# Kernel tuning notes

Hardware: AMD Instinct MI355X
Metric: run time of the kernel (lower is better)

The kernel has to match this reference:

```python
import jax, jax.numpy as jnp
import numpy as np

B, T, D, I, E, R = 4, 2048, 2048, 6144, 8, 32


def setup_inputs() -> dict:
    key = jax.random.key(0)
    ks = jax.random.split(key, 9)
    return {
        "x": jax.random.normal(ks[0], (B, T, D), jnp.float32),
        "router_w": jax.random.normal(ks[1], (D, E), jnp.float32) * 0.02,
        "A_gate": jax.random.normal(ks[2], (E, D, R), jnp.float32) * 0.01,
        "B_gate": jax.random.normal(ks[3], (E, R, I), jnp.float32) * 0.01,
        "A_up": jax.random.normal(ks[4], (E, D, R), jnp.float32) * 0.01,
        "B_up": jax.random.normal(ks[5], (E, R, I), jnp.float32) * 0.01,
        "W_gate": jax.random.normal(ks[6], (D, I), jnp.float32) * 0.02,
        "W_up": jax.random.normal(ks[7], (D, I), jnp.float32) * 0.02,
        "W_down": jax.random.normal(ks[8], (I, D), jnp.float32) * 0.02,
    }


def reference(x, router_w, A_gate, B_gate, A_up, B_up, W_gate, W_up, W_down):
    b, t, d = x.shape
    flat = x.reshape(b * t, d)                     # [N, D]
    # Router: top-1 expert per token (argmax matches torch argmax: first max)
    gate_logits = flat @ router_w                  # [N, E]
    idx = jnp.argmax(gate_logits, axis=-1)         # [N]
    n_exp = router_w.shape[1]

    def routed_lora(A, Bm):
        # sum_e mask_e * (x @ A_e @ B_e); loop over small static expert count
        out = jnp.zeros((flat.shape[0], Bm.shape[2]), flat.dtype)
        for e in range(n_exp):
            m = (idx == e)[:, None]
            out = out + jnp.where(m, (flat @ A[e]) @ Bm[e], 0.0)
        return out

    # ExpertLoRA forward: base gate/up + per-token-selected LoRA delta, SwiGLU, down
    gate = flat @ W_gate + routed_lora(A_gate, B_gate)   # [N, I]
    up = flat @ W_up + routed_lora(A_up, B_up)           # [N, I]
    down = (jax.nn.silu(gate) * up) @ W_down             # [N, D]
    return down.reshape(b, t, d), gate_logits
```

## Files before the change

kernel.cpp:

```cpp
#include <hip/hip_runtime.h>
#include <stdint.h>

#define N_TOK 8192
#define DDIM 2048
#define IDIM 6144
#define NEXP 8
#define RLORA 32
#define NCHUNK 64
#define CHUNK 128

typedef __attribute__((ext_vector_type(8))) short short8;
typedef __attribute__((ext_vector_type(4))) float floatx4;
typedef __attribute__((ext_vector_type(4))) unsigned short ushortx4;

__device__ __forceinline__ unsigned short f2bf(float f) {
  union { float f; unsigned u; } v; v.f = f;
  unsigned u = v.u;
  unsigned r = (u + 0x7fffu + ((u >> 16) & 1u)) >> 16;
  return (unsigned short)r;
}
__device__ __forceinline__ float bf2f(unsigned short s) {
  union { unsigned u; float f; } v; v.u = ((unsigned)s) << 16;
  return v.f;
}

__device__ __forceinline__ void gload_lds16(const void* g, void* l) {
  __builtin_amdgcn_global_load_lds(
      (const __attribute__((address_space(1))) void*)g,
      (__attribute__((address_space(3))) void*)l, 16, 0, 0);
}

__global__ __launch_bounds__(256) void router_kernel(
    const float* __restrict__ x, const float* __restrict__ rw,
    float* __restrict__ logits_out, int* __restrict__ idx) {
  int wave = threadIdx.x >> 6, lane = threadIdx.x & 63;
  int n = blockIdx.x * 4 + wave;
  const float* xr = x + (size_t)n * DDIM;
  float acc[NEXP];
#pragma unroll
  for (int e = 0; e < NEXP; e++) acc[e] = 0.f;
#pragma unroll
  for (int j = 0; j < 8; j++) {
    int d = j * 256 + lane * 4;
    floatx4 v = *(const floatx4*)(xr + d);
    const float* rwd = rw + (size_t)d * NEXP;
#pragma unroll
    for (int t = 0; t < 4; t++) {
      float xv = v[t];
      const float* rr = rwd + t * NEXP;
#pragma unroll
      for (int e = 0; e < NEXP; e++) acc[e] += xv * rr[e];
    }
  }
#pragma unroll
  for (int off = 32; off > 0; off >>= 1) {
#pragma unroll
    for (int e = 0; e < NEXP; e++) acc[e] += __shfl_xor(acc[e], off, 64);
  }
  if (lane == 0) {
    float best = acc[0]; int bi = 0;
#pragma unroll
    for (int e = 1; e < NEXP; e++)
      if (acc[e] > best) { best = acc[e]; bi = e; }
    idx[n] = bi;
#pragma unroll
    for (int e = 0; e < NEXP; e++) logits_out[(size_t)n * NEXP + e] = acc[e];
  }
}

__global__ __launch_bounds__(128) void count_kernel(
    const int* __restrict__ idx, int* __restrict__ cnt) {
  __shared__ int h[NEXP];
  if (threadIdx.x < NEXP) h[threadIdx.x] = 0;
  __syncthreads();
  int n = blockIdx.x * CHUNK + threadIdx.x;
  atomicAdd(&h[idx[n]], 1);
  __syncthreads();
  if (threadIdx.x < NEXP) cnt[blockIdx.x * NEXP + threadIdx.x] = h[threadIdx.x];
}

__global__ __launch_bounds__(64) void scan_kernel(
    const int* __restrict__ cnt, int* __restrict__ off) {
  __shared__ int tot[NEXP], base[NEXP];
  int t = threadIdx.x;
  if (t < NEXP) {
    int s = 0;
    for (int c = 0; c < NCHUNK; c++) s += cnt[c * NEXP + t];
    tot[t] = s;
  }
  __syncthreads();
  if (t == 0) {
    int run = 0;
    for (int e = 0; e < NEXP; e++) { base[e] = run; run += tot[e]; }
  }
  __syncthreads();
  if (t < NEXP) {
    int run = base[t];
    for (int c = 0; c < NCHUNK; c++) { off[c * NEXP + t] = run; run += cnt[c * NEXP + t]; }
  }
}

__global__ __launch_bounds__(64) void rank_kernel(
    const int* __restrict__ idx, const int* __restrict__ off,
    int* __restrict__ sortpos, int* __restrict__ orig, int* __restrict__ eidx) {
  if (threadIdx.x != 0) return;
  int c = blockIdx.x;
  int lc[NEXP];
#pragma unroll
  for (int e = 0; e < NEXP; e++) lc[e] = 0;
  for (int t = 0; t < CHUNK; t++) {
    int n = c * CHUNK + t;
    int e = idx[n];
    int dst = off[c * NEXP + e] + lc[e]++;
    sortpos[n] = dst;
    orig[dst] = n;
    eidx[dst] = e;
  }
}

__global__ __launch_bounds__(256) void permute_x_kernel(
    const float* __restrict__ x, const int* __restrict__ sortpos,
    unsigned short* __restrict__ xb) {
  int wave = threadIdx.x >> 6, lane = threadIdx.x & 63;
  int n = blockIdx.x * 4 + wave;
  int dst = sortpos[n];
  const float* xr = x + (size_t)n * DDIM;
  unsigned short* xbr = xb + (size_t)dst * DDIM;
#pragma unroll
  for (int j = 0; j < 8; j++) {
    int d = j * 256 + lane * 4;
    floatx4 v = *(const floatx4*)(xr + d);
    ushortx4 s;
    s[0] = f2bf(v[0]); s[1] = f2bf(v[1]); s[2] = f2bf(v[2]); s[3] = f2bf(v[3]);
    *(ushortx4*)(xbr + d) = s;
  }
}

__global__ __launch_bounds__(256) void transpose_w_kernel(
    const float* __restrict__ in, unsigned short* __restrict__ out, int Rr, int Cc) {
  __shared__ float lds[32][33];
  int r0 = blockIdx.y * 32, c0 = blockIdx.x * 32;
  int tx = threadIdx.x & 31, ty = threadIdx.x >> 5;
#pragma unroll
  for (int k = 0; k < 4; k++) {
    int r = ty + k * 8;
    lds[r][tx] = in[(size_t)(r0 + r) * Cc + c0 + tx];
  }
  __syncthreads();
#pragma unroll
  for (int k = 0; k < 4; k++) {
    int cc = ty + k * 8;
    out[(size_t)(c0 + cc) * Rr + r0 + tx] = f2bf(lds[tx][cc]);
  }
}

__global__ __launch_bounds__(256) void pack_a_kernel(
    const float* __restrict__ Ag, const float* __restrict__ Au,
    unsigned short* __restrict__ aat) {
  int o = blockIdx.x * 256 + threadIdx.x;
  int h = o >> 19;
  int oo = o & ((1 << 19) - 1);
  int c = oo >> 11, d = oo & 2047;
  int e = c >> 5, r = c & 31;
  const float* src = h ? Au : Ag;
  float v = src[(e << 16) + (d << 5) + r];
  aat[(size_t)(h * 256 + c) * DDIM + d] = f2bf(v);
}

__global__ __launch_bounds__(256) void transpose_b_kernel(
    const float* __restrict__ Bg, const float* __restrict__ Bu,
    unsigned short* __restrict__ btg, unsigned short* __restrict__ btu) {
  __shared__ float lds[32][33];
  int i0 = blockIdx.x * 32, e = blockIdx.y;
  const float* in = blockIdx.z ? Bu : Bg;
  unsigned short* out = blockIdx.z ? btu : btg;
  int tx = threadIdx.x & 31, ty = threadIdx.x >> 5;
#pragma unroll
  for (int k = 0; k < 4; k++) {
    int r = ty + k * 8;
    lds[r][tx] = in[((size_t)e * RLORA + r) * IDIM + i0 + tx];
  }
  __syncthreads();
#pragma unroll
  for (int k = 0; k < 4; k++) {
    int ii = ty + k * 8;
    out[((size_t)e * IDIM + i0 + ii) * RLORA + tx] = f2bf(lds[tx][ii]);
  }
}

__global__ __launch_bounds__(256) void gemm_tsel_kernel(
    const unsigned short* __restrict__ xb, const unsigned short* __restrict__ aat,
    const int* __restrict__ eidx, unsigned short* __restrict__ Tsel) {
  __shared__ __align__(16) unsigned short sA[4096], sB[2048];
  __shared__ int es_s[128];
  const int row0 = blockIdx.x * 128;
  const int tid = threadIdx.x;
  const int wave = tid >> 6, lane = tid & 63;
  const int wr = wave >> 1, wc = wave & 1;
  const int q = lane >> 4, m16 = lane & 15;
  if (tid < 128) es_s[tid] = eidx[row0 + tid];
  __syncthreads();
  const int emin = es_s[0], emax = es_s[127];
  int erow[4];
#pragma unroll
  for (int m = 0; m < 4; m++) erow[m] = es_s[wr * 64 + m * 16 + m16];
  floatx4 acc[8];
#pragma unroll
  for (int i = 0; i < 8; i++)
#pragma unroll
    for (int j = 0; j < 4; j++) acc[i][j] = 0.f;
  short8 zero;
#pragma unroll
  for (int i = 0; i < 8; i++) zero[i] = 0;
  for (int ee = emin; ee <= emax; ee++) {
    for (int k0 = 0; k0 < DDIM; k0 += 32) {
      __syncthreads();
#pragma unroll
      for (int rr = 0; rr < 2; rr++) {
        int e = tid * 8 + rr * 2048;
        int r = e >> 5, kk = e & 31;
        gload_lds16(xb + (size_t)(row0 + r) * DDIM + (k0 + kk), sA + e);
      }
      {
        int e2 = tid * 8;
        int c = e2 >> 5, kk = e2 & 31;
        int srow = (c < 32) ? (ee * 32 + c) : (256 + ee * 32 + (c - 32));
        gload_lds16(aat + (size_t)srow * DDIM + (k0 + kk), sB + e2);
      }
      __syncthreads();
      short8 a[4], b[2];
#pragma unroll
      for (int m = 0; m < 4; m++) {
        short8 av = *(const short8*)(sA + (wr * 64 + m * 16 + m16) * 32 + q * 8);
        a[m] = (erow[m] == ee) ? av : zero;
      }
#pragma unroll
      for (int n = 0; n < 2; n++)
        b[n] = *(const short8*)(sB + (wc * 32 + n * 16 + m16) * 32 + q * 8);
#pragma unroll
      for (int m = 0; m < 4; m++)
#pragma unroll
        for (int n = 0; n < 2; n++)
          acc[m * 2 + n] = __builtin_amdgcn_mfma_f32_16x16x32_bf16(a[m], b[n], acc[m * 2 + n], 0, 0, 0);
    }
  }
#pragma unroll
  for (int m = 0; m < 4; m++)
#pragma unroll
    for (int n = 0; n < 2; n++)
#pragma unroll
      for (int r = 0; r < 4; r++) {
        int grow = row0 + wr * 64 + m * 16 + q * 4 + r;
        int gcol = wc * 32 + n * 16 + m16;
        Tsel[(size_t)grow * 64 + gcol] = f2bf(acc[m * 2 + n][r]);
      }
}

__device__ __forceinline__ void mm_main(const unsigned short* __restrict__ Ab,
                                        const unsigned short* __restrict__ Bb,
                                        int K, int row0, int col0,
                                        unsigned short* sA, unsigned short* sB,
                                        floatx4* acc) {
  const int tid = threadIdx.x;
  const int wave = tid >> 6, lane = tid & 63;
  const int wr = wave >> 1, wc = wave & 1;
  const int q = lane >> 4, m16 = lane & 15;
  for (int k0 = 0; k0 < K; k0 += 32) {
    __syncthreads();
#pragma unroll
    for (int rr = 0; rr < 2; rr++) {
      int e = tid * 8 + rr * 2048;
      int r = e >> 5, kk = e & 31;
      gload_lds16(Ab + (size_t)(row0 + r) * K + (k0 + kk), sA + e);
      gload_lds16(Bb + (size_t)(col0 + r) * K + (k0 + kk), sB + e);
    }
    __syncthreads();
    short8 a[4], b[4];
#pragma unroll
    for (int m = 0; m < 4; m++)
      a[m] = *(const short8*)(sA + (wr * 64 + m * 16 + m16) * 32 + q * 8);
#pragma unroll
    for (int n = 0; n < 4; n++)
      b[n] = *(const short8*)(sB + (wc * 64 + n * 16 + m16) * 32 + q * 8);
#pragma unroll
    for (int m = 0; m < 4; m++)
#pragma unroll
      for (int n = 0; n < 4; n++)
        acc[m * 4 + n] = __builtin_amdgcn_mfma_f32_16x16x32_bf16(a[m], b[n], acc[m * 4 + n], 0, 0, 0);
  }
}

__device__ __forceinline__ void lora_epilogue(const unsigned short* __restrict__ Tsel,
                                              const unsigned short* __restrict__ Bt,
                                              const int* __restrict__ eidx,
                                              int half, int row0, int col0,
                                              unsigned short* sA, unsigned short* sB,
                                              int* es_s, floatx4* acc) {
  const int tid = threadIdx.x;
  const int wave = tid >> 6, lane = tid & 63;
  const int wr = wave >> 1, wc = wave & 1;
  const int q = lane >> 4, m16 = lane & 15;
  __syncthreads();
  if (tid < 128) es_s[tid] = eidx[row0 + tid];
#pragma unroll
  for (int rr = 0; rr < 2; rr++) {
    int e = tid * 8 + rr * 2048;
    int r = e >> 5, kk = e & 31;
    *(floatx4*)(sA + e) = *(const floatx4*)(Tsel + (size_t)(row0 + r) * 64 + half * 32 + kk);
  }
  __syncthreads();
  const int emin = es_s[0], emax = es_s[127];
  short8 ta[4]; int erow[4];
#pragma unroll
  for (int m = 0; m < 4; m++) {
    int rloc = wr * 64 + m * 16 + m16;
    ta[m] = *(const short8*)(sA + rloc * 32 + q * 8);
    erow[m] = es_s[rloc];
  }
  short8 zero;
#pragma unroll
  for (int i = 0; i < 8; i++) zero[i] = 0;
  for (int ee = emin; ee <= emax; ee++) {
    __syncthreads();
#pragma unroll
    for (int rr = 0; rr < 2; rr++) {
      int e2 = tid * 8 + rr * 2048;
      int c = e2 >> 5, kk = e2 & 31;
      *(floatx4*)(sB + e2) = *(const floatx4*)(Bt + ((size_t)ee * IDIM + col0 + c) * RLORA + kk);
    }
    __syncthreads();
    short8 bfr[4];
#pragma unroll
    for (int n = 0; n < 4; n++)
      bfr[n] = *(const short8*)(sB + (wc * 64 + n * 16 + m16) * 32 + q * 8);
#pragma unroll
    for (int m = 0; m < 4; m++) {
      short8 am = (erow[m] == ee) ? ta[m] : zero;
#pragma unroll
      for (int n = 0; n < 4; n++)
        acc[m * 4 + n] = __builtin_amdgcn_mfma_f32_16x16x32_bf16(am, bfr[n], acc[m * 4 + n], 0, 0, 0);
    }
  }
}

__device__ __forceinline__ void swizzle_gu(int lin, int& bx, int& by) {
  int xcd = lin & 7, slot = lin >> 3;
  bx = xcd * 6 + slot % 6;
  by = slot / 6;
}

__global__ __launch_bounds__(256) void gemm_gate_kernel(
    const unsigned short* __restrict__ xb, const unsigned short* __restrict__ wgt,
    const unsigned short* __restrict__ Tsel, const unsigned short* __restrict__ btg,
    const int* __restrict__ eidx, unsigned short* __restrict__ gbuf) {
  __shared__ __align__(16) unsigned short sA[4096], sB[4096];
  __shared__ int es_s[128];
  floatx4 acc[16];
#pragma unroll
  for (int i = 0; i < 16; i++)
#pragma unroll
    for (int j = 0; j < 4; j++) acc[i][j] = 0.f;
  int bx, by; swizzle_gu(blockIdx.x, bx, by);
  int row0 = by * 128, col0 = bx * 128;
  mm_main(xb, wgt, DDIM, row0, col0, sA, sB, acc);
  lora_epilogue(Tsel, btg, eidx, 0, row0, col0, sA, sB, es_s, acc);
  const int wave = threadIdx.x >> 6, lane = threadIdx.x & 63;
  const int wr = wave >> 1, wc = wave & 1;
  const int q = lane >> 4, m16 = lane & 15;
#pragma unroll
  for (int m = 0; m < 4; m++)
#pragma unroll
    for (int n = 0; n < 4; n++)
#pragma unroll
      for (int r = 0; r < 4; r++) {
        int grow = row0 + wr * 64 + m * 16 + q * 4 + r;
        int gcol = col0 + wc * 64 + n * 16 + m16;
        gbuf[(size_t)grow * IDIM + gcol] = f2bf(acc[m * 4 + n][r]);
      }
}

__global__ __launch_bounds__(256) void gemm_up_kernel(
    const unsigned short* __restrict__ xb, const unsigned short* __restrict__ wut,
    const unsigned short* __restrict__ Tsel, const unsigned short* __restrict__ btu,
    const int* __restrict__ eidx, unsigned short* __restrict__ gbuf) {
  __shared__ __align__(16) unsigned short sA[4096], sB[4096];
  __shared__ int es_s[128];
  floatx4 acc[16];
#pragma unroll
  for (int i = 0; i < 16; i++)
#pragma unroll
    for (int j = 0; j < 4; j++) acc[i][j] = 0.f;
  int bx, by; swizzle_gu(blockIdx.x, bx, by);
  int row0 = by * 128, col0 = bx * 128;
  mm_main(xb, wut, DDIM, row0, col0, sA, sB, acc);
  lora_epilogue(Tsel, btu, eidx, 1, row0, col0, sA, sB, es_s, acc);
  const int wave = threadIdx.x >> 6, lane = threadIdx.x & 63;
  const int wr = wave >> 1, wc = wave & 1;
  const int q = lane >> 4, m16 = lane & 15;
#pragma unroll
  for (int m = 0; m < 4; m++)
#pragma unroll
    for (int n = 0; n < 4; n++)
#pragma unroll
      for (int r = 0; r < 4; r++) {
        int grow = row0 + wr * 64 + m * 16 + q * 4 + r;
        int gcol = col0 + wc * 64 + n * 16 + m16;
        size_t o = (size_t)grow * IDIM + gcol;
        float gv = bf2f(gbuf[o]);
        float hv = gv / (1.f + __expf(-gv)) * acc[m * 4 + n][r];
        gbuf[o] = f2bf(hv);
      }
}

__global__ __launch_bounds__(256) void gemm_down_kernel(
    const unsigned short* __restrict__ hb, const unsigned short* __restrict__ wdt,
    const int* __restrict__ orig, float* __restrict__ out) {
  __shared__ __align__(16) unsigned short sA[4096], sB[4096];
  floatx4 acc[16];
#pragma unroll
  for (int i = 0; i < 16; i++)
#pragma unroll
    for (int j = 0; j < 4; j++) acc[i][j] = 0.f;
  int lin = blockIdx.x;
  int xcd = lin & 7, slot = lin >> 3;
  int bx = xcd * 2 + (slot & 1);
  int by = slot >> 1;
  int row0 = by * 128, col0 = bx * 128;
  mm_main(hb, wdt, IDIM, row0, col0, sA, sB, acc);
  const int wave = threadIdx.x >> 6, lane = threadIdx.x & 63;
  const int wr = wave >> 1, wc = wave & 1;
  const int q = lane >> 4, m16 = lane & 15;
#pragma unroll
  for (int m = 0; m < 4; m++)
#pragma unroll
    for (int n = 0; n < 4; n++)
#pragma unroll
      for (int r = 0; r < 4; r++) {
        int grow = row0 + wr * 64 + m * 16 + q * 4 + r;
        int orow = orig[grow];
        int gcol = col0 + wc * 64 + n * 16 + m16;
        out[(size_t)orow * DDIM + gcol] = acc[m * 4 + n][r];
      }
}

extern "C" void kernel_launch(void* const* d_in, const int* in_sizes, int n_in,
                              void* d_out, int out_size, void* d_ws, size_t ws_size,
                              hipStream_t stream) {
  const float* x  = (const float*)d_in[0];
  const float* rw = (const float*)d_in[1];
  const float* Ag = (const float*)d_in[2];
  const float* Bg = (const float*)d_in[3];
  const float* Au = (const float*)d_in[4];
  const float* Bu = (const float*)d_in[5];
  const float* Wg = (const float*)d_in[6];
  const float* Wu = (const float*)d_in[7];
  const float* Wd = (const float*)d_in[8];
  float* out = (float*)d_out;
  float* logits = out + (size_t)N_TOK * DDIM;

  char* ws = (char*)d_ws;
  size_t off = 0;
  auto alloc = [&](size_t bytes) {
    char* p = ws + off;
    off += (bytes + 255) & ~(size_t)255;
    return p;
  };
  unsigned short* xb  = (unsigned short*)alloc((size_t)N_TOK * DDIM * 2);
  unsigned short* wgt = (unsigned short*)alloc((size_t)IDIM * DDIM * 2);
  unsigned short* wut = (unsigned short*)alloc((size_t)IDIM * DDIM * 2);
  unsigned short* wdt = (unsigned short*)alloc((size_t)DDIM * IDIM * 2);
  unsigned short* aat = (unsigned short*)alloc((size_t)512 * DDIM * 2);
  unsigned short* btg = (unsigned short*)alloc((size_t)NEXP * IDIM * RLORA * 2);
  unsigned short* btu = (unsigned short*)alloc((size_t)NEXP * IDIM * RLORA * 2);
  unsigned short* Tsel= (unsigned short*)alloc((size_t)N_TOK * 64 * 2);
  unsigned short* gbuf= (unsigned short*)alloc((size_t)N_TOK * IDIM * 2);
  int* idx     = (int*)alloc((size_t)N_TOK * 4);
  int* sortpos = (int*)alloc((size_t)N_TOK * 4);
  int* orig    = (int*)alloc((size_t)N_TOK * 4);
  int* eidx    = (int*)alloc((size_t)N_TOK * 4);
  int* cnt     = (int*)alloc((size_t)NCHUNK * NEXP * 4);
  int* offb    = (int*)alloc((size_t)NCHUNK * NEXP * 4);

  router_kernel<<<N_TOK / 4, 256, 0, stream>>>(x, rw, logits, idx);
  count_kernel<<<NCHUNK, 128, 0, stream>>>(idx, cnt);
  scan_kernel<<<1, 64, 0, stream>>>(cnt, offb);
  rank_kernel<<<NCHUNK, 64, 0, stream>>>(idx, offb, sortpos, orig, eidx);
  permute_x_kernel<<<N_TOK / 4, 256, 0, stream>>>(x, sortpos, xb);
  transpose_w_kernel<<<dim3(IDIM / 32, DDIM / 32), 256, 0, stream>>>(Wg, wgt, DDIM, IDIM);
  transpose_w_kernel<<<dim3(IDIM / 32, DDIM / 32), 256, 0, stream>>>(Wu, wut, DDIM, IDIM);
  transpose_w_kernel<<<dim3(DDIM / 32, IDIM / 32), 256, 0, stream>>>(Wd, wdt, IDIM, DDIM);
  pack_a_kernel<<<4096, 256, 0, stream>>>(Ag, Au, aat);
  transpose_b_kernel<<<dim3(IDIM / 32, NEXP, 2), 256, 0, stream>>>(Bg, Bu, btg, btu);
  gemm_tsel_kernel<<<N_TOK / 128, 256, 0, stream>>>(xb, aat, eidx, Tsel);
  gemm_gate_kernel<<<(IDIM / 128) * (N_TOK / 128), 256, 0, stream>>>(xb, wgt, Tsel, btg, eidx, gbuf);
  gemm_up_kernel<<<(IDIM / 128) * (N_TOK / 128), 256, 0, stream>>>(xb, wut, Tsel, btu, eidx, gbuf);
  gemm_down_kernel<<<(DDIM / 128) * (N_TOK / 128), 256, 0, stream>>>(gbuf, wdt, orig, out);
}
```

Baseline: 1.238 ms.

## Fuse gate and up GEMMs with LoRA and SwiGLU into one kernel

Replaces the separate gate and up GEMM kernels with one kernel. Each 128x64 output tile computes both gate and up accumulators from a shared x tile, applies the routed LoRA deltas for both, and writes silu(gate)*up directly. This removes the bf16 round-trip of the gate intermediate through global memory and halves the x-tile loads. The cost is more registers per thread and narrower N tiles, with launch_bounds set to allow 3 blocks per CU.

Result: no change. 1.215 ms (-1.9%).

```diff
diff --git a/kernel.cpp b/kernel.cpp
--- a/kernel.cpp
+++ b/kernel.cpp
@@ -18,10 +18,6 @@
   unsigned u = v.u;
   unsigned r = (u + 0x7fffu + ((u >> 16) & 1u)) >> 16;
   return (unsigned short)r;
-}
-__device__ __forceinline__ float bf2f(unsigned short s) {
-  union { unsigned u; float f; } v; v.u = ((unsigned)s) << 16;
-  return v.f;
 }
 
 __device__ __forceinline__ void gload_lds16(const void* g, void* l) {
@@ -256,6 +252,133 @@
       }
 }
 
+__global__ __launch_bounds__(256, 3) void gemm_gateup_kernel(
+    const unsigned short* __restrict__ xb, const unsigned short* __restrict__ wgt,
+    const unsigned short* __restrict__ wut, const unsigned short* __restrict__ Tsel,
+    const unsigned short* __restrict__ btg, const unsigned short* __restrict__ btu,
+    const int* __restrict__ eidx, unsigned short* __restrict__ hbuf) {
+  __shared__ __align__(16) unsigned short smem[12288];
+  __shared__ int es_s[128];
+  unsigned short* sA  = smem;
+  unsigned short* sBg = smem + 4096;
+  unsigned short* sBu = smem + 6144;
+  unsigned short* sTg = smem;
+  unsigned short* sTu = smem + 4096;
+  unsigned short* sbg = smem + 8192;
+  unsigned short* sbu = smem + 10240;
+
+  floatx4 accg[8], accu[8];
+#pragma unroll
+  for (int i = 0; i < 8; i++)
+#pragma unroll
+    for (int j = 0; j < 4; j++) { accg[i][j] = 0.f; accu[i][j] = 0.f; }
+
+  int lin = blockIdx.x;
+  int xcd = lin & 7, slot = lin >> 3;
+  int grp = slot >> 8, sub = slot & 255;
+  int bx = xcd * 12 + grp * 4 + (sub & 3);
+  int by = sub >> 2;
+  const int row0 = by * 128, col0 = bx * 64;
+
+  const int tid = threadIdx.x;
+  const int wave = tid >> 6, lane = tid & 63;
+  const int wr = wave >> 1, wc = wave & 1;
+  const int q = lane >> 4, m16 = lane & 15;
+
+  for (int k0 = 0; k0 < DDIM; k0 += 32) {
+    __syncthreads();
+#pragma unroll
+    for (int rr = 0; rr < 2; rr++) {
+      int e = tid * 8 + rr * 2048;
+      int r = e >> 5, kk = e & 31;
+      gload_lds16(xb + (size_t)(row0 + r) * DDIM + (k0 + kk), sA + e);
+    }
+    {
+      int e2 = tid * 8;
+      int c = e2 >> 5, kk = e2 & 31;
+      gload_lds16(wgt + (size_t)(col0 + c) * DDIM + (k0 + kk), sBg + e2);
+      gload_lds16(wut + (size_t)(col0 + c) * DDIM + (k0 + kk), sBu + e2);
+    }
+    __syncthreads();
+    short8 a[4], bg[2], bu[2];
+#pragma unroll
+    for (int m = 0; m < 4; m++)
+      a[m] = *(const short8*)(sA + (wr * 64 + m * 16 + m16) * 32 + q * 8);
+#pragma unroll
+    for (int n = 0; n < 2; n++) {
+      bg[n] = *(const short8*)(sBg + (wc * 32 + n * 16 + m16) * 32 + q * 8);
+      bu[n] = *(const short8*)(sBu + (wc * 32 + n * 16 + m16) * 32 + q * 8);
+    }
+#pragma unroll
+    for (int m = 0; m < 4; m++)
+#pragma unroll
+      for (int n = 0; n < 2; n++) {
+        accg[m * 2 + n] = __builtin_amdgcn_mfma_f32_16x16x32_bf16(a[m], bg[n], accg[m * 2 + n], 0, 0, 0);
+        accu[m * 2 + n] = __builtin_amdgcn_mfma_f32_16x16x32_bf16(a[m], bu[n], accu[m * 2 + n], 0, 0, 0);
+      }
+  }
+
+  __syncthreads();
+  if (tid < 128) es_s[tid] = eidx[row0 + tid];
+#pragma unroll
+  for (int rr = 0; rr < 2; rr++) {
+    int e = tid * 8 + rr * 2048;
+    int r = e >> 5, kk = e & 31;
+    *(floatx4*)(sTg + e) = *(const floatx4*)(Tsel + (size_t)(row0 + r) * 64 + kk);
+    *(floatx4*)(sTu + e) = *(const floatx4*)(Tsel + (size_t)(row0 + r) * 64 + 32 + kk);
+  }
+  __syncthreads();
+  const int emin = es_s[0], emax = es_s[127];
+  int erow[4];
+#pragma unroll
+  for (int m = 0; m < 4; m++) erow[m] = es_s[wr * 64 + m * 16 + m16];
+  short8 zero;
+#pragma unroll
+  for (int i = 0; i < 8; i++) zero[i] = 0;
+  for (int ee = emin; ee <= emax; ee++) {
+    __syncthreads();
+    {
+      int e2 = tid * 8;
+      int c = e2 >> 5, kk = e2 & 31;
+      *(floatx4*)(sbg + e2) = *(const floatx4*)(btg + ((size_t)ee * IDIM + col0 + c) * RLORA + kk);
+      *(floatx4*)(sbu + e2) = *(const floatx4*)(btu + ((size_t)ee * IDIM + col0 + c) * RLORA + kk);
+    }
+    __syncthreads();
+    short8 bg[2], bu[2], tg[4], tu[4];
+#pragma unroll
+    for (int n = 0; n < 2; n++) {
+      bg[n] = *(const short8*)(sbg + (wc * 32 + n * 16 + m16) * 32 + q * 8);
+      bu[n] = *(const short8*)(sbu + (wc * 32 + n * 16 + m16) * 32 + q * 8);
+    }
+#pragma unroll
+    for (int m = 0; m < 4; m++) {
+      int rloc = wr * 64 + m * 16 + m16;
+      tg[m] = (erow[m] == ee) ? *(const short8*)(sTg + rloc * 32 + q * 8) : zero;
+      tu[m] = (erow[m] == ee) ? *(const short8*)(sTu + rloc * 32 + q * 8) : zero;
+    }
+#pragma unroll
+    for (int m = 0; m < 4; m++)
+#pragma unroll
+      for (int n = 0; n < 2; n++) {
+        accg[m * 2 + n] = __builtin_amdgcn_mfma_f32_16x16x32_bf16(tg[m], bg[n], accg[m * 2 + n], 0, 0, 0);
+        accu[m * 2 + n] = __builtin_amdgcn_mfma_f32_16x16x32_bf16(tu[m], bu[n], accu[m * 2 + n], 0, 0, 0);
+      }
+  }
+
+#pragma unroll
+  for (int m = 0; m < 4; m++)
+#pragma unroll
+    for (int n = 0; n < 2; n++)
+#pragma unroll
+      for (int r = 0; r < 4; r++) {
+        int grow = row0 + wr * 64 + m * 16 + q * 4 + r;
+        int gcol = col0 + wc * 32 + n * 16 + m16;
+        float gv = accg[m * 2 + n][r];
+        float hv = gv / (1.f + __expf(-gv)) * accu[m * 2 + n][r];
+        hbuf[(size_t)grow * IDIM + gcol] = f2bf(hv);
+      }
+}
+
 __device__ __forceinline__ void mm_main(const unsigned short* __restrict__ Ab,
                                         const unsigned short* __restrict__ Bb,
                                         int K, int row0, int col0,
@@ -288,128 +411,6 @@
       for (int n = 0; n < 4; n++)
         acc[m * 4 + n] = __builtin_amdgcn_mfma_f32_16x16x32_bf16(a[m], b[n], acc[m * 4 + n], 0, 0, 0);
   }
-}
-
-__device__ __forceinline__ void lora_epilogue(const unsigned short* __restrict__ Tsel,
-                                              const unsigned short* __restrict__ Bt,
-                                              const int* __restrict__ eidx,
-                                              int half, int row0, int col0,
-                                              unsigned short* sA, unsigned short* sB,
-                                              int* es_s, floatx4* acc) {
-  const int tid = threadIdx.x;
-  const int wave = tid >> 6, lane = tid & 63;
-  const int wr = wave >> 1, wc = wave & 1;
-  const int q = lane >> 4, m16 = lane & 15;
-  __syncthreads();
-  if (tid < 128) es_s[tid] = eidx[row0 + tid];
-#pragma unroll
-  for (int rr = 0; rr < 2; rr++) {
-    int e = tid * 8 + rr * 2048;
-    int r = e >> 5, kk = e & 31;
-    *(floatx4*)(sA + e) = *(const floatx4*)(Tsel + (size_t)(row0 + r) * 64 + half * 32 + kk);
-  }
-  __syncthreads();
-  const int emin = es_s[0], emax = es_s[127];
-  short8 ta[4]; int erow[4];
-#pragma unroll
-  for (int m = 0; m < 4; m++) {
-    int rloc = wr * 64 + m * 16 + m16;
-    ta[m] = *(const short8*)(sA + rloc * 32 + q * 8);
-    erow[m] = es_s[rloc];
-  }
-  short8 zero;
-#pragma unroll
-  for (int i = 0; i < 8; i++) zero[i] = 0;
-  for (int ee = emin; ee <= emax; ee++) {
-    __syncthreads();
-#pragma unroll
-    for (int rr = 0; rr < 2; rr++) {
-      int e2 = tid * 8 + rr * 2048;
-      int c = e2 >> 5, kk = e2 & 31;
-      *(floatx4*)(sB + e2) = *(const floatx4*)(Bt + ((size_t)ee * IDIM + col0 + c) * RLORA + kk);
-    }
-    __syncthreads();
-    short8 bfr[4];
-#pragma unroll
-    for (int n = 0; n < 4; n++)
-      bfr[n] = *(const short8*)(sB + (wc * 64 + n * 16 + m16) * 32 + q * 8);
-#pragma unroll
-    for (int m = 0; m < 4; m++) {
-      short8 am = (erow[m] == ee) ? ta[m] : zero;
-#pragma unroll
-      for (int n = 0; n < 4; n++)
-        acc[m * 4 + n] = __builtin_amdgcn_mfma_f32_16x16x32_bf16(am, bfr[n], acc[m * 4 + n], 0, 0, 0);
-    }
-  }
-}
-
-__device__ __forceinline__ void swizzle_gu(int lin, int& bx, int& by) {
-  int xcd = lin & 7, slot = lin >> 3;
-  bx = xcd * 6 + slot % 6;
-  by = slot / 6;
-}
-
-__global__ __launch_bounds__(256) void gemm_gate_kernel(
-    const unsigned short* __restrict__ xb, const unsigned short* __restrict__ wgt,
-    const unsigned short* __restrict__ Tsel, const unsigned short* __restrict__ btg,
-    const int* __restrict__ eidx, unsigned short* __restrict__ gbuf) {
-  __shared__ __align__(16) unsigned short sA[4096], sB[4096];
-  __shared__ int es_s[128];
-  floatx4 acc[16];
-#pragma unroll
-  for (int i = 0; i < 16; i++)
-#pragma unroll
-    for (int j = 0; j < 4; j++) acc[i][j] = 0.f;
-  int bx, by; swizzle_gu(blockIdx.x, bx, by);
-  int row0 = by * 128, col0 = bx * 128;
-  mm_main(xb, wgt, DDIM, row0, col0, sA, sB, acc);
-  lora_epilogue(Tsel, btg, eidx, 0, row0, col0, sA, sB, es_s, acc);
-  const int wave = threadIdx.x >> 6, lane = threadIdx.x & 63;
-  const int wr = wave >> 1, wc = wave & 1;
-  const int q = lane >> 4, m16 = lane & 15;
-#pragma unroll
-  for (int m = 0; m < 4; m++)
-#pragma unroll
-    for (int n = 0; n < 4; n++)
-#pragma unroll
-      for (int r = 0; r < 4; r++) {
-        int grow = row0 + wr * 64 + m * 16 + q * 4 + r;
-        int gcol = col0 + wc * 64 + n * 16 + m16;
-        gbuf[(size_t)grow * IDIM + gcol] = f2bf(acc[m * 4 + n][r]);
-      }
-}
-
-__global__ __launch_bounds__(256) void gemm_up_kernel(
-    const unsigned short* __restrict__ xb, const unsigned short* __restrict__ wut,
-    const unsigned short* __restrict__ Tsel, const unsigned short* __restrict__ btu,
-    const int* __restrict__ eidx, unsigned short* __restrict__ gbuf) {
-  __shared__ __align__(16) unsigned short sA[4096], sB[4096];
-  __shared__ int es_s[128];
-  floatx4 acc[16];
-#pragma unroll
-  for (int i = 0; i < 16; i++)
-#pragma unroll
-    for (int j = 0; j < 4; j++) acc[i][j] = 0.f;
-  int bx, by; swizzle_gu(blockIdx.x, bx, by);
-  int row0 = by * 128, col0 = bx * 128;
-  mm_main(xb, wut, DDIM, row0, col0, sA, sB, acc);
-  lora_epilogue(Tsel, btu, eidx, 1, row0, col0, sA, sB, es_s, acc);
-  const int wave = threadIdx.x >> 6, lane = threadIdx.x & 63;
-  const int wr = wave >> 1, wc = wave & 1;
-  const int q = lane >> 4, m16 = lane & 15;
-#pragma unroll
-  for (int m = 0; m < 4; m++)
-#pragma unroll
-    for (int n = 0; n < 4; n++)
-#pragma unroll
-      for (int r = 0; r < 4; r++) {
-        int grow = row0 + wr * 64 + m * 16 + q * 4 + r;
-        int gcol = col0 + wc * 64 + n * 16 + m16;
-        size_t o = (size_t)grow * IDIM + gcol;
-        float gv = bf2f(gbuf[o]);
-        float hv = gv / (1.f + __expf(-gv)) * acc[m * 4 + n][r];
-        gbuf[o] = f2bf(hv);
-      }
 }
 
 __global__ __launch_bounds__(256) void gemm_down_kernel(
@@ -473,7 +474,7 @@
   unsigned short* btg = (unsigned short*)alloc((size_t)NEXP * IDIM * RLORA * 2);
   unsigned short* btu = (unsigned short*)alloc((size_t)NEXP * IDIM * RLORA * 2);
   unsigned short* Tsel= (unsigned short*)alloc((size_t)N_TOK * 64 * 2);
-  unsigned short* gbuf= (unsigned short*)alloc((size_t)N_TOK * IDIM * 2);
+  unsigned short* hbuf= (unsigned short*)alloc((size_t)N_TOK * IDIM * 2);
   int* idx     = (int*)alloc((size_t)N_TOK * 4);
   int* sortpos = (int*)alloc((size_t)N_TOK * 4);
   int* orig    = (int*)alloc((size_t)N_TOK * 4);
@@ -492,7 +493,7 @@
   pack_a_kernel<<<4096, 256, 0, stream>>>(Ag, Au, aat);
   transpose_b_kernel<<<dim3(IDIM / 32, NEXP, 2), 256, 0, stream>>>(Bg, Bu, btg, btu);
   gemm_tsel_kernel<<<N_TOK / 128, 256, 0, stream>>>(xb, aat, eidx, Tsel);
-  gemm_gate_kernel<<<(IDIM / 128) * (N_TOK / 128), 256, 0, stream>>>(xb, wgt, Tsel, btg, eidx, gbuf);
-  gemm_up_kernel<<<(IDIM / 128) * (N_TOK / 128), 256, 0, stream>>>(xb, wut, Tsel, btu, eidx, gbuf);
-  gemm_down_kernel<<<(DDIM / 128) * (N_TOK / 128), 256, 0, stream>>>(gbuf, wdt, orig, out);
-}
+  gemm_gateup_kernel<<<(IDIM / 64) * (N_TOK / 128), 256, 0, stream>>>(
+      xb, wgt, wut, Tsel, btg, btu, eidx, hbuf);
+  gemm_down_kernel<<<(DDIM / 128) * (N_TOK / 128), 256, 0, stream>>>(hbuf, wdt, orig, out);
+}
```
